# Performance work log

Hardware: AMD Instinct MI355X
Metric: run time of the kernel (lower is better)

Reference implementation:

```python
import jax, jax.numpy as jnp
import numpy as np

EMBED = 256
HEADS = 8
HD = EMBED // HEADS          # head_dim = key_dim = 32 (value_factor=1)
SCALE = HD ** (-0.5)


def angle_transform(x, sin, cos):
    # x: (b, nh, h, w, hd); sin/cos broadcast over leading dims
    x1 = x[..., ::2]
    x2 = x[..., 1::2]
    rot = jnp.stack([-x2, x1], axis=-1).reshape(x.shape)  # interleave (-x2, x1)
    return x * cos + rot * sin


def setup_inputs() -> dict:
    key = jax.random.key(0)
    ks = jax.random.split(key, 12)
    B, H, W = 4, 48, 48
    x = jax.random.normal(ks[0], (B, H, W, EMBED), jnp.float32)
    ang = jax.random.normal(ks[1], (H, W, HD), jnp.float32)
    sin = jnp.sin(ang)
    cos = jnp.cos(ang)
    mask = jax.random.normal(ks[2], (HEADS, H * W, H * W), jnp.float32) * 0.1
    s = 0.05
    Wq = jax.random.normal(ks[3], (EMBED, EMBED), jnp.float32) * s
    bq = jnp.zeros((EMBED,), jnp.float32)
    Wk = jax.random.normal(ks[4], (EMBED, EMBED), jnp.float32) * s
    bk = jnp.zeros((EMBED,), jnp.float32)
    Wv = jax.random.normal(ks[5], (EMBED, EMBED), jnp.float32) * s
    bv = jnp.zeros((EMBED,), jnp.float32)
    lepe_w = jax.random.normal(ks[6], (5, 5, 1, EMBED), jnp.float32) * 0.1  # HWIO, depthwise
    lepe_b = jnp.zeros((EMBED,), jnp.float32)
    Wout = jax.random.normal(ks[7], (EMBED, EMBED), jnp.float32) * s
    bout = jnp.zeros((EMBED,), jnp.float32)
    return {"x": x, "sin": sin, "cos": cos, "mask": mask,
            "Wq": Wq, "bq": bq, "Wk": Wk, "bk": bk, "Wv": Wv, "bv": bv,
            "lepe_w": lepe_w, "lepe_b": lepe_b, "Wout": Wout, "bout": bout}


def reference(x, sin, cos, mask, Wq, bq, Wk, bk, Wv, bv, lepe_w, lepe_b, Wout, bout):
    B, H, W, C = x.shape
    q = x @ Wq + bq
    k = (x @ Wk + bk) * SCALE
    v = x @ Wv + bv
    # depthwise 5x5 conv (lepe) on v, NHWC
    lepe = jax.lax.conv_general_dilated(
        v, lepe_w, window_strides=(1, 1), padding=[(2, 2), (2, 2)],
        dimension_numbers=("NHWC", "HWIO", "NHWC"), feature_group_count=C) + lepe_b
    qh = q.reshape(B, H, W, HEADS, HD).transpose(0, 3, 1, 2, 4)  # (b,nh,h,w,hd)
    kh = k.reshape(B, H, W, HEADS, HD).transpose(0, 3, 1, 2, 4)
    qr = angle_transform(qh, sin, cos).reshape(B, HEADS, H * W, HD)
    kr = angle_transform(kh, sin, cos).reshape(B, HEADS, H * W, HD)
    vr = v.reshape(B, H, W, HEADS, -1).transpose(0, 3, 1, 2, 4).reshape(B, HEADS, H * W, -1)
    attn = jax.nn.softmax(jnp.einsum("bnqd,bnkd->bnqk", qr, kr) + mask, axis=-1)
    out = jnp.einsum("bnqk,bnkd->bnqd", attn, vr)
    out = out.transpose(0, 2, 1, 3).reshape(B, H, W, -1) + lepe
    return out @ Wout + bout
```

## Files before the change

### kernel.cpp

```cpp
#include <hip/hip_runtime.h>
#include <hip/hip_bf16.h>
#include <math.h>

constexpr int kB     = 4;
constexpr int kH     = 48;
constexpr int kW     = 48;
constexpr int kHW    = 2304;
constexpr int kC     = 256;
constexpr int kHeads = 8;
constexpr int kHD    = 32;
constexpr float kScale = 0.17677669529663687f;

typedef __bf16 bf16x8 __attribute__((ext_vector_type(8)));
typedef float  f32x4  __attribute__((ext_vector_type(4)));
typedef unsigned int   uint32x4 __attribute__((ext_vector_type(4)));
typedef unsigned short ushort8v __attribute__((ext_vector_type(8)));

static __device__ __forceinline__ unsigned short f2bf_bits(float f) {
    return __builtin_bit_cast(unsigned short, __float2bfloat16(f));
}

static __device__ __forceinline__ unsigned cvt_pk_bf16(float lo, float hi) {
    unsigned r;
    asm("v_cvt_pk_bf16_f32 %0, %1, %2" : "=v"(r) : "v"(lo), "v"(hi));
    return r;
}

static __device__ __forceinline__ void permlane16_swap(unsigned& a, unsigned& b) {
    asm("v_permlane16_swap_b32 %0, %1" : "+v"(a), "+v"(b));
}
static __device__ __forceinline__ void permlane32_swap(unsigned& a, unsigned& b) {
    asm("v_permlane32_swap_b32 %0, %1" : "+v"(a), "+v"(b));
}

static __device__ __forceinline__ void gll16(const void* g, void* l) {
    __builtin_amdgcn_global_load_lds(
        (const __attribute__((address_space(1))) void*)g,
        (__attribute__((address_space(3))) void*)l, 16, 0, 0);
}

__global__ __launch_bounds__(256) void prep_kernel(
    const float* __restrict__ x,
    const float* __restrict__ Wq, const float* __restrict__ Wk,
    const float* __restrict__ Wv, const float* __restrict__ Wo,
    unsigned short* __restrict__ xb, unsigned short* __restrict__ wt)
{
    const int bid = blockIdx.x;
    if (bid < 2304) {
        const int i = (bid * 256 + threadIdx.x) * 4;
        const float4 v = *reinterpret_cast<const float4*>(x + i);
        alignas(8) unsigned short u[4] = {f2bf_bits(v.x), f2bf_bits(v.y),
                                          f2bf_bits(v.z), f2bf_bits(v.w)};
        *reinterpret_cast<unsigned long long*>(xb + i) =
            *reinterpret_cast<unsigned long long*>(u);
    } else {
        const int e = (bid - 2304) * 256 + threadIdx.x;
        const int m = e >> 16;
        const int r = e & 65535;
        const int k = r >> 8;
        const int n = r & 255;
        const float* W = (m == 0) ? Wq : ((m == 1) ? Wk : ((m == 2) ? Wv : Wo));
        wt[(size_t)m * 65536 + n * 256 + k] = f2bf_bits(W[k * 256 + n]);
    }
}

__global__ __launch_bounds__(256) void qkv_mfma_kernel(
    const unsigned short* __restrict__ xb, const unsigned short* __restrict__ wt,
    const float* __restrict__ bq, const float* __restrict__ bk,
    const float* __restrict__ bv,
    const float* __restrict__ sinb, const float* __restrict__ cosb,
    unsigned short* __restrict__ qbh, unsigned short* __restrict__ kbh,
    unsigned short* __restrict__ vt, float* __restrict__ vb)
{
    const int z = blockIdx.z;
    const unsigned short* wz = wt + (size_t)z * 65536;
    const float* bt = (z == 0) ? bq : ((z == 1) ? bk : bv);
    const int tid  = threadIdx.x;
    const int w    = tid >> 6;
    const int lane = tid & 63;
    const int l    = lane & 15;
    const int g    = lane >> 4;
    const int m0   = blockIdx.x * 64 + w * 16;
    const int nb   = blockIdx.y * 64;

    f32x4 acc[4] = {};
    const unsigned short* xrow = xb + (size_t)(m0 + l) * 256;
    #pragma unroll
    for (int kc = 0; kc < 8; ++kc) {
        const bf16x8 a = *reinterpret_cast<const bf16x8*>(xrow + kc * 32 + g * 8);
        #pragma unroll
        for (int j = 0; j < 4; ++j) {
            const bf16x8 b = *reinterpret_cast<const bf16x8*>(
                wz + (size_t)(nb + 16 * j + l) * 256 + kc * 32 + g * 8);
            acc[j] = __builtin_amdgcn_mfma_f32_16x16x32_bf16(a, b, acc[j], 0, 0, 0);
        }
    }

    int tok[4], bidx[4], hw[4];
    #pragma unroll
    for (int r = 0; r < 4; ++r) {
        tok[r]  = m0 + 4 * g + r;
        bidx[r] = tok[r] / kHW;
        hw[r]   = tok[r] - bidx[r] * kHW;
    }
    const float scl = (z == 1) ? kScale : 1.0f;

    if (z == 2) {
        #pragma unroll
        for (int j = 0; j < 4; ++j) {
            const int c = nb + 16 * j + l;
            const int head = c >> 5, d = c & 31;
            const float bias = bt[c];
            float t[4];
            #pragma unroll
            for (int r = 0; r < 4; ++r) t[r] = acc[j][r] + bias;
            #pragma unroll
            for (int r = 0; r < 4; ++r)
                vb[(((size_t)(bidx[r] * kHeads + head) * kHW + hw[r]) << 5) + d] = t[r];
            alignas(8) unsigned short u[4] = {f2bf_bits(t[0]), f2bf_bits(t[1]),
                                              f2bf_bits(t[2]), f2bf_bits(t[3])};
            *reinterpret_cast<unsigned long long*>(
                vt + ((size_t)(bidx[0] * kHeads + head) * kHD + d) * kHW + hw[0]) =
                *reinterpret_cast<unsigned long long*>(u);
        }
    } else {
        unsigned short* ob = (z == 0) ? qbh : kbh;
        #pragma unroll
        for (int j = 0; j < 4; ++j) {
            const int c = nb + 16 * j + l;
            const int head = c >> 5, d = c & 31;
            const float bias = bt[c];
            float t[4];
            #pragma unroll
            for (int r = 0; r < 4; ++r) t[r] = (acc[j][r] + bias) * scl;
            #pragma unroll
            for (int r = 0; r < 4; ++r) {
                const float p = __shfl_xor(t[r], 1);
                const float cs = cosb[hw[r] * 32 + d];
                const float sn = sinb[hw[r] * 32 + d];
                const float o = (d & 1) ? (t[r] * cs + p * sn)
                                        : (t[r] * cs - p * sn);
                ob[(((size_t)(bidx[r] * kHeads + head) * kHW + hw[r]) << 5) + d] =
                    f2bf_bits(o);
            }
        }
    }
}

__global__ __launch_bounds__(256) void lepe_kernel(
    const float* __restrict__ vb,
    const float* __restrict__ lw, const float* __restrict__ lb,
    float* __restrict__ lepe)
{
    const int c   = threadIdx.x;
    const int bhw = blockIdx.x;
    const int b   = bhw / kHW;
    const int hw  = bhw % kHW;
    const int h   = hw / kW;
    const int w   = hw % kW;
    const int head = c >> 5;
    const int d    = c & 31;

    const float* vsrc = vb + ((size_t)(b * kHeads + head) * kHW) * kHD + d;
    float acc = lb[c];
    #pragma unroll
    for (int dh = 0; dh < 5; ++dh) {
        const int h2 = h + dh - 2;
        if (h2 < 0 || h2 >= kH) continue;
        #pragma unroll
        for (int dw = 0; dw < 5; ++dw) {
            const int w2 = w + dw - 2;
            if (w2 < 0 || w2 >= kW) continue;
            acc += vsrc[(size_t)(h2 * kW + w2) * kHD] * lw[(dh * 5 + dw) * kC + c];
        }
    }
    lepe[(size_t)bhw * kC + c] = acc;
}

__global__ __launch_bounds__(512, 4) void attn_mfma_kernel(
    const __hip_bfloat16* __restrict__ qb, const __hip_bfloat16* __restrict__ kb,
    const __hip_bfloat16* __restrict__ vt, const float* __restrict__ mask,
    float* __restrict__ po, float* __restrict__ ls, int kspan)
{
    extern __shared__ __align__(16) char smem[];
    constexpr int kBufStride = 40960;
    constexpr int kKOff = 8192;
    constexpr int kVOff = 24576;

    const int head = blockIdx.y;
    const int ksl  = blockIdx.z;
    const int tid  = threadIdx.x;
    const int w    = tid >> 6;
    const int b    = w & 3;
    const int sh   = w >> 2;
    const int bh   = b * kHeads + head;
    const int lane = tid & 63;
    const int lq   = lane & 15;
    const int g    = lane >> 4;
    const int q0   = blockIdx.x * 32;
    const int kt0  = ksl * kspan;
    const int nt   = kspan >> 6;
    const bool odd16 = (g & 1);

    const bf16x8 qfrag = *reinterpret_cast<const bf16x8*>(
        reinterpret_cast<const unsigned short*>(qb) +
        ((size_t)bh * kHW + q0 + 16 * sh + lq) * kHD + g * 8);

    const float* msrc;
    {
        const int mrow = w * 4 + (lane >> 4);
        const int mcb  = (lane & 15) ^ (mrow & 7);
        msrc = mask + ((size_t)head * kHW + q0 + mrow) * kHW + kt0 + mcb * 4;
    }
    const unsigned short* kvsrc[4];
    int kvstep, kvregion;
    {
        const unsigned short* kb_bh =
            reinterpret_cast<const unsigned short*>(kb) + (size_t)bh * kHW * kHD;
        const unsigned short* vt_bh =
            reinterpret_cast<const unsigned short*>(vt) + (size_t)bh * kHD * kHW;
        if (sh == 0) {
            #pragma unroll
            for (int i = 0; i < 4; ++i) {
                const int key   = i * 16 + (lane >> 2);
                const int kslot = (lane & 3) ^ (key & 3);
                kvsrc[i] = kb_bh + (size_t)(kt0 + key) * kHD + kslot * 8;
            }
            kvstep = 64 * kHD;
            kvregion = kKOff;
        } else {
            #pragma unroll
            for (int i = 0; i < 4; ++i) {
                const int d   = i * 8 + (lane >> 3);
                const int vcu = (lane & 7) ^ (d & 7);
                kvsrc[i] = vt_bh + (size_t)d * kHW + kt0 + vcu * 8;
            }
            kvstep = 64;
            kvregion = kVOff;
        }
    }

    auto STAGE = [&](int bufo, int tt) {
        gll16(msrc + (size_t)tt * 64, smem + bufo + w * 1024);
        char* kv = smem + bufo + kvregion + b * 4096;
        #pragma unroll
        for (int i = 0; i < 4; ++i)
            gll16(kvsrc[i] + (size_t)tt * kvstep, kv + i * 1024);
    };

    f32x4 o0 = {0.f, 0.f, 0.f, 0.f};
    f32x4 o1 = {0.f, 0.f, 0.f, 0.f};
    float lsum = 0.f;

    const int koff = lq * 64 + ((g ^ (lq & 3)) * 16);
    const int vxa  = (g ^ (lq & 7)) * 16;
    const int vxb  = ((4 + g) ^ (lq & 7)) * 16;

    STAGE(0, 0);

    int cur = 0;
    for (int t = 0; t < nt; ++t) {
        if (t + 1 < nt) {
            STAGE(cur ^ kBufStride, t + 1);
            asm volatile("s_waitcnt vmcnt(5)" ::: "memory");
        } else {
            asm volatile("s_waitcnt vmcnt(0)" ::: "memory");
        }
        __builtin_amdgcn_s_barrier();
        __builtin_amdgcn_sched_barrier(0);

        const char* mb  = smem + cur;
        const char* kbf = smem + cur + kKOff + b * 4096;
        const char* vbf = smem + cur + kVOff + b * 4096;

        bf16x8 kf[4];
        #pragma unroll
        for (int j = 0; j < 4; ++j)
            kf[j] = *reinterpret_cast<const bf16x8*>(kbf + j * 1024 + koff);
        const bf16x8 va  = *reinterpret_cast<const bf16x8*>(vbf + lq * 128 + vxa);
        const bf16x8 vb2 = *reinterpret_cast<const bf16x8*>(vbf + lq * 128 + vxb);
        const bf16x8 vc  = *reinterpret_cast<const bf16x8*>(vbf + (16 + lq) * 128 + vxa);
        const bf16x8 vd  = *reinterpret_cast<const bf16x8*>(vbf + (16 + lq) * 128 + vxb);

        f32x4 st[4];
        #pragma unroll
        for (int j = 0; j < 4; ++j) {
            const f32x4 mc = *reinterpret_cast<const f32x4*>(
                mb + sh * 4096 + lq * 256 + (((4 * j + g) ^ (lq & 7)) * 16));
            st[j] = __builtin_amdgcn_mfma_f32_16x16x32_bf16(kf[j], qfrag, mc, 0, 0, 0);
        }

        unsigned p32[4][2];
        #pragma unroll
        for (int j = 0; j < 4; ++j) {
            const float e0 = __expf(st[j][0]);
            const float e1 = __expf(st[j][1]);
            const float e2 = __expf(st[j][2]);
            const float e3 = __expf(st[j][3]);
            lsum += (e0 + e1) + (e2 + e3);
            p32[j][0] = cvt_pk_bf16(e0, e1);
            p32[j][1] = cvt_pk_bf16(e2, e3);
        }

        unsigned sj[4][2][2];
        #pragma unroll
        for (int j = 0; j < 4; ++j)
            #pragma unroll
            for (int r = 0; r < 2; ++r) {
                unsigned a = p32[j][r], b2 = p32[j][r];
                permlane16_swap(a, b2);
                sj[j][r][0] = a; sj[j][r][1] = b2;
            }
        unsigned pw0[4], pw1[4];
        #pragma unroll
        for (int w2 = 0; w2 < 4; ++w2) {
            const int r = w2 & 1, c = w2 >> 1;
            unsigned pa = sj[0][r][c], pb = sj[1][r][c];
            permlane32_swap(pa, pb);
            pw0[w2] = odd16 ? pb : pa;
            unsigned qa = sj[2][r][c], qb2 = sj[3][r][c];
            permlane32_swap(qa, qb2);
            pw1[w2] = odd16 ? qb2 : qa;
        }
        uint32x4 w0v = {pw0[0], pw0[1], pw0[2], pw0[3]};
        uint32x4 w1v = {pw1[0], pw1[1], pw1[2], pw1[3]};
        const bf16x8 pa0 = __builtin_bit_cast(bf16x8, w0v);
        const bf16x8 pa1 = __builtin_bit_cast(bf16x8, w1v);

        o0 = __builtin_amdgcn_mfma_f32_16x16x32_bf16(pa0, va,  o0, 0, 0, 0);
        o0 = __builtin_amdgcn_mfma_f32_16x16x32_bf16(pa1, vb2, o0, 0, 0, 0);
        o1 = __builtin_amdgcn_mfma_f32_16x16x32_bf16(pa0, vc,  o1, 0, 0, 0);
        o1 = __builtin_amdgcn_mfma_f32_16x16x32_bf16(pa1, vd,  o1, 0, 0, 0);

        asm volatile("s_waitcnt lgkmcnt(0)" ::: "memory");
        __builtin_amdgcn_s_barrier();
        cur ^= kBufStride;
    }

    lsum += __shfl_xor(lsum, 16);
    lsum += __shfl_xor(lsum, 32);

    const size_t pbase = ((size_t)ksl * (kB * kHeads) + bh) * kHW;
    #pragma unroll
    for (int r = 0; r < 4; ++r) {
        float* orow = po + (pbase + q0 + 16 * sh + 4 * g + r) * kHD + lq;
        orow[0]  = o0[r];
        orow[16] = o1[r];
    }
    if (lane < 16) ls[pbase + q0 + 16 * sh + lq] = lsum;
}

__global__ __launch_bounds__(256) void combine_kernel(
    const float* __restrict__ po, const float* __restrict__ ls,
    const float* __restrict__ lepe, unsigned short* __restrict__ abh, int ks)
{
    const int idx = blockIdx.x * 256 + threadIdx.x;
    const int c   = idx & 255;
    const int bhw = idx >> 8;
    const int b   = bhw / kHW;
    const int hw  = bhw % kHW;
    const int head = c >> 5;
    const int d    = c & 31;
    const int bh   = b * kHeads + head;

    float o = 0.f, l = 0.f;
    for (int s = 0; s < ks; ++s) {
        const size_t pbase = ((size_t)s * (kB * kHeads) + bh) * kHW + hw;
        o += po[pbase * kHD + d];
        l += ls[pbase];
    }
    abh[(size_t)idx] = f2bf_bits(o / l + lepe[idx]);
}

__global__ __launch_bounds__(256) void out_mfma_kernel(
    const unsigned short* __restrict__ abh, const unsigned short* __restrict__ wt,
    const float* __restrict__ bo, float* __restrict__ out)
{
    const unsigned short* wz = wt + (size_t)3 * 65536;
    const int tid  = threadIdx.x;
    const int w    = tid >> 6;
    const int lane = tid & 63;
    const int l    = lane & 15;
    const int g    = lane >> 4;
    const int m0   = blockIdx.x * 64 + w * 16;
    const int nb   = blockIdx.y * 64;

    f32x4 acc[4] = {};
    const unsigned short* arow = abh + (size_t)(m0 + l) * 256;
    #pragma unroll
    for (int kc = 0; kc < 8; ++kc) {
        const bf16x8 a = *reinterpret_cast<const bf16x8*>(arow + kc * 32 + g * 8);
        #pragma unroll
        for (int j = 0; j < 4; ++j) {
            const bf16x8 b = *reinterpret_cast<const bf16x8*>(
                wz + (size_t)(nb + 16 * j + l) * 256 + kc * 32 + g * 8);
            acc[j] = __builtin_amdgcn_mfma_f32_16x16x32_bf16(a, b, acc[j], 0, 0, 0);
        }
    }

    #pragma unroll
    for (int j = 0; j < 4; ++j) {
        const int c = nb + 16 * j + l;
        const float bias = bo[c];
        #pragma unroll
        for (int r = 0; r < 4; ++r)
            out[(size_t)(m0 + 4 * g + r) * 256 + c] = acc[j][r] + bias;
    }
}

extern "C" void kernel_launch(void* const* d_in, const int* in_sizes, int n_in,
                              void* d_out, int out_size, void* d_ws, size_t ws_size,
                              hipStream_t stream)
{
    const float* x    = (const float*)d_in[0];
    const float* sinb = (const float*)d_in[1];
    const float* cosb = (const float*)d_in[2];
    const float* mask = (const float*)d_in[3];
    const float* Wq   = (const float*)d_in[4];
    const float* bq   = (const float*)d_in[5];
    const float* Wk   = (const float*)d_in[6];
    const float* bk   = (const float*)d_in[7];
    const float* Wv   = (const float*)d_in[8];
    const float* bv   = (const float*)d_in[9];
    const float* lw   = (const float*)d_in[10];
    const float* lb   = (const float*)d_in[11];
    const float* Wo   = (const float*)d_in[12];
    const float* bo   = (const float*)d_in[13];
    float* out = (float*)d_out;

    const size_t NT = (size_t)kB * kHeads * kHW * kHD;
    const size_t fixed = NT * 4 * 2 + NT * 2 * 5 + 4 * 65536 * 2;

    int ks = 4;
    while (ks > 1) {
        const size_t need = fixed + (size_t)ks * (NT * 4 + (size_t)kB * kHeads * kHW * 4);
        if (need <= ws_size) break;
        ks >>= 1;
    }
    const int kspan = kHW / ks;

    char* base = (char*)d_ws;
    float* vb   = (float*)base;                      base += NT * 4;
    float* lepe = (float*)base;                      base += NT * 4;
    unsigned short* xb  = (unsigned short*)base;     base += NT * 2;
    unsigned short* abh = (unsigned short*)base;     base += NT * 2;
    unsigned short* qbh = (unsigned short*)base;     base += NT * 2;
    unsigned short* kbh = (unsigned short*)base;     base += NT * 2;
    unsigned short* vt  = (unsigned short*)base;     base += NT * 2;
    unsigned short* wt  = (unsigned short*)base;     base += (size_t)4 * 65536 * 2;
    float* po = (float*)base;                        base += (size_t)ks * NT * 4;
    float* ls = (float*)base;                        base += (size_t)ks * kB * kHeads * kHW * 4;

    prep_kernel<<<dim3(3328), 256, 0, stream>>>(x, Wq, Wk, Wv, Wo, xb, wt);
    qkv_mfma_kernel<<<dim3(144, 4, 3), 256, 0, stream>>>(
        xb, wt, bq, bk, bv, sinb, cosb, qbh, kbh, vt, vb);
    lepe_kernel<<<dim3(9216), 256, 0, stream>>>(vb, lw, lb, lepe);
    attn_mfma_kernel<<<dim3(72, 8, ks), 512, 81920, stream>>>(
        (const __hip_bfloat16*)qbh, (const __hip_bfloat16*)kbh,
        (const __hip_bfloat16*)vt, mask, po, ls, kspan);
    combine_kernel<<<dim3(9216), 256, 0, stream>>>(po, ls, lepe, abh, ks);
    out_mfma_kernel<<<dim3(144, 4), 256, 0, stream>>>(abh, wt, bo, out);
}
```

Baseline: 186.5 us.

## Halve attention key tile to 32 and cut LDS, split-K, and raise occupancy

The attention kernel now processes 32 keys per iteration instead of 64, halving the LDS buffer to 40 KB so more blocks can reside per CU (launch bounds raised to 8). Staging is split so one half of the waves loads mask and K while the other loads V, and s_setprio brackets the MFMA section. The split-K factor drops from 4 to 2, which shrinks the partial-output traffic and the combine work but gives each block twice as many iterations. The smaller tile doubles the number of barriers per key processed and gives less MFMA work between them.

Result: slower. 190.6 us (+2.2%).

```diff
diff --git a/kernel.cpp b/kernel.cpp
--- a/kernel.cpp
+++ b/kernel.cpp
@@ -177,15 +177,15 @@
     lepe[(size_t)bhw * kC + c] = acc;
 }
 
-__global__ __launch_bounds__(512, 4) void attn_mfma_kernel(
+__global__ __launch_bounds__(512, 8) void attn_mfma_kernel(
     const __hip_bfloat16* __restrict__ qb, const __hip_bfloat16* __restrict__ kb,
     const __hip_bfloat16* __restrict__ vt, const float* __restrict__ mask,
     float* __restrict__ po, float* __restrict__ ls, int kspan)
 {
     extern __shared__ __align__(16) char smem[];
-    constexpr int kBufStride = 40960;
-    constexpr int kKOff = 8192;
-    constexpr int kVOff = 24576;
+    constexpr int kBufStride = 20480;
+    constexpr int kKOff = 4096;
+    constexpr int kVOff = 12288;
 
     const int head = blockIdx.y;
     const int ksl  = blockIdx.z;
@@ -199,62 +199,60 @@
     const int g    = lane >> 4;
     const int q0   = blockIdx.x * 32;
     const int kt0  = ksl * kspan;
-    const int nt   = kspan >> 6;
+    const int nt   = kspan >> 5;
     const bool odd16 = (g & 1);
 
     const bf16x8 qfrag = *reinterpret_cast<const bf16x8*>(
         reinterpret_cast<const unsigned short*>(qb) +
         ((size_t)bh * kHW + q0 + 16 * sh + lq) * kHD + g * 8);
 
-    const float* msrc;
-    {
-        const int mrow = w * 4 + (lane >> 4);
-        const int mcb  = (lane & 15) ^ (mrow & 7);
-        msrc = mask + ((size_t)head * kHW + q0 + mrow) * kHW + kt0 + mcb * 4;
-    }
-    const unsigned short* kvsrc[4];
-    int kvstep, kvregion;
+    const float* msrc = nullptr;
+    const unsigned short* kvsrc[2];
     {
         const unsigned short* kb_bh =
             reinterpret_cast<const unsigned short*>(kb) + (size_t)bh * kHW * kHD;
         const unsigned short* vt_bh =
             reinterpret_cast<const unsigned short*>(vt) + (size_t)bh * kHD * kHW;
         if (sh == 0) {
-            #pragma unroll
-            for (int i = 0; i < 4; ++i) {
+            const int mrow = w * 8 + (lane >> 3);
+            const int mslot = (lane & 7) ^ (mrow & 7);
+            msrc = mask + ((size_t)head * kHW + q0 + mrow) * kHW + kt0 + mslot * 4;
+            #pragma unroll
+            for (int i = 0; i < 2; ++i) {
                 const int key   = i * 16 + (lane >> 2);
                 const int kslot = (lane & 3) ^ (key & 3);
                 kvsrc[i] = kb_bh + (size_t)(kt0 + key) * kHD + kslot * 8;
             }
-            kvstep = 64 * kHD;
-            kvregion = kKOff;
         } else {
             #pragma unroll
-            for (int i = 0; i < 4; ++i) {
-                const int d   = i * 8 + (lane >> 3);
-                const int vcu = (lane & 7) ^ (d & 7);
-                kvsrc[i] = vt_bh + (size_t)d * kHW + kt0 + vcu * 8;
+            for (int i = 0; i < 2; ++i) {
+                const int d    = i * 16 + (lane >> 2);
+                const int vslot = (lane & 3) ^ (d & 3);
+                kvsrc[i] = vt_bh + (size_t)d * kHW + kt0 + vslot * 8;
             }
-            kvstep = 64;
-            kvregion = kVOff;
         }
     }
 
     auto STAGE = [&](int bufo, int tt) {
-        gll16(msrc + (size_t)tt * 64, smem + bufo + w * 1024);
-        char* kv = smem + bufo + kvregion + b * 4096;
-        #pragma unroll
-        for (int i = 0; i < 4; ++i)
-            gll16(kvsrc[i] + (size_t)tt * kvstep, kv + i * 1024);
+        if (sh == 0) {
+            gll16(msrc + (size_t)tt * 32, smem + bufo + w * 1024);
+            #pragma unroll
+            for (int i = 0; i < 2; ++i)
+                gll16(kvsrc[i] + (size_t)tt * 1024,
+                      smem + bufo + kKOff + b * 2048 + i * 1024);
+        } else {
+            #pragma unroll
+            for (int i = 0; i < 2; ++i)
+                gll16(kvsrc[i] + (size_t)tt * 32,
+                      smem + bufo + kVOff + b * 2048 + i * 1024);
+        }
     };
 
     f32x4 o0 = {0.f, 0.f, 0.f, 0.f};
     f32x4 o1 = {0.f, 0.f, 0.f, 0.f};
     float lsum = 0.f;
 
-    const int koff = lq * 64 + ((g ^ (lq & 3)) * 16);
-    const int vxa  = (g ^ (lq & 7)) * 16;
-    const int vxb  = ((4 + g) ^ (lq & 7)) * 16;
+    const int kvx = (g ^ (lq & 3)) * 16;
 
     STAGE(0, 0);
 
@@ -262,7 +260,8 @@
     for (int t = 0; t < nt; ++t) {
         if (t + 1 < nt) {
             STAGE(cur ^ kBufStride, t + 1);
-            asm volatile("s_waitcnt vmcnt(5)" ::: "memory");
+            if (sh == 0) asm volatile("s_waitcnt vmcnt(3)" ::: "memory");
+            else         asm volatile("s_waitcnt vmcnt(2)" ::: "memory");
         } else {
             asm volatile("s_waitcnt vmcnt(0)" ::: "memory");
         }
@@ -270,29 +269,28 @@
         __builtin_amdgcn_sched_barrier(0);
 
         const char* mb  = smem + cur;
-        const char* kbf = smem + cur + kKOff + b * 4096;
-        const char* vbf = smem + cur + kVOff + b * 4096;
-
-        bf16x8 kf[4];
-        #pragma unroll
-        for (int j = 0; j < 4; ++j)
-            kf[j] = *reinterpret_cast<const bf16x8*>(kbf + j * 1024 + koff);
-        const bf16x8 va  = *reinterpret_cast<const bf16x8*>(vbf + lq * 128 + vxa);
-        const bf16x8 vb2 = *reinterpret_cast<const bf16x8*>(vbf + lq * 128 + vxb);
-        const bf16x8 vc  = *reinterpret_cast<const bf16x8*>(vbf + (16 + lq) * 128 + vxa);
-        const bf16x8 vd  = *reinterpret_cast<const bf16x8*>(vbf + (16 + lq) * 128 + vxb);
-
-        f32x4 st[4];
-        #pragma unroll
-        for (int j = 0; j < 4; ++j) {
+        const char* kbf = smem + cur + kKOff + b * 2048;
+        const char* vbf = smem + cur + kVOff + b * 2048;
+
+        bf16x8 kf[2];
+        #pragma unroll
+        for (int j = 0; j < 2; ++j)
+            kf[j] = *reinterpret_cast<const bf16x8*>(kbf + (16 * j + lq) * 64 + kvx);
+        const bf16x8 va = *reinterpret_cast<const bf16x8*>(vbf + lq * 64 + kvx);
+        const bf16x8 vc = *reinterpret_cast<const bf16x8*>(vbf + (16 + lq) * 64 + kvx);
+
+        __builtin_amdgcn_s_setprio(1);
+        f32x4 st[2];
+        #pragma unroll
+        for (int j = 0; j < 2; ++j) {
             const f32x4 mc = *reinterpret_cast<const f32x4*>(
-                mb + sh * 4096 + lq * 256 + (((4 * j + g) ^ (lq & 7)) * 16));
+                mb + (16 * sh + lq) * 128 + (((4 * j + g) ^ (lq & 7)) * 16));
             st[j] = __builtin_amdgcn_mfma_f32_16x16x32_bf16(kf[j], qfrag, mc, 0, 0, 0);
         }
 
-        unsigned p32[4][2];
-        #pragma unroll
-        for (int j = 0; j < 4; ++j) {
+        unsigned p32[2][2];
+        #pragma unroll
+        for (int j = 0; j < 2; ++j) {
             const float e0 = __expf(st[j][0]);
             const float e1 = __expf(st[j][1]);
             const float e2 = __expf(st[j][2]);
@@ -302,35 +300,29 @@
             p32[j][1] = cvt_pk_bf16(e2, e3);
         }
 
-        unsigned sj[4][2][2];
-        #pragma unroll
-        for (int j = 0; j < 4; ++j)
+        unsigned sj[2][2][2];
+        #pragma unroll
+        for (int j = 0; j < 2; ++j)
             #pragma unroll
             for (int r = 0; r < 2; ++r) {
                 unsigned a = p32[j][r], b2 = p32[j][r];
                 permlane16_swap(a, b2);
                 sj[j][r][0] = a; sj[j][r][1] = b2;
             }
-        unsigned pw0[4], pw1[4];
+        unsigned pw0[4];
         #pragma unroll
         for (int w2 = 0; w2 < 4; ++w2) {
             const int r = w2 & 1, c = w2 >> 1;
             unsigned pa = sj[0][r][c], pb = sj[1][r][c];
             permlane32_swap(pa, pb);
             pw0[w2] = odd16 ? pb : pa;
-            unsigned qa = sj[2][r][c], qb2 = sj[3][r][c];
-            permlane32_swap(qa, qb2);
-            pw1[w2] = odd16 ? qb2 : qa;
         }
         uint32x4 w0v = {pw0[0], pw0[1], pw0[2], pw0[3]};
-        uint32x4 w1v = {pw1[0], pw1[1], pw1[2], pw1[3]};
         const bf16x8 pa0 = __builtin_bit_cast(bf16x8, w0v);
-        const bf16x8 pa1 = __builtin_bit_cast(bf16x8, w1v);
-
-        o0 = __builtin_amdgcn_mfma_f32_16x16x32_bf16(pa0, va,  o0, 0, 0, 0);
-        o0 = __builtin_amdgcn_mfma_f32_16x16x32_bf16(pa1, vb2, o0, 0, 0, 0);
-        o1 = __builtin_amdgcn_mfma_f32_16x16x32_bf16(pa0, vc,  o1, 0, 0, 0);
-        o1 = __builtin_amdgcn_mfma_f32_16x16x32_bf16(pa1, vd,  o1, 0, 0, 0);
+
+        o0 = __builtin_amdgcn_mfma_f32_16x16x32_bf16(pa0, va, o0, 0, 0, 0);
+        o1 = __builtin_amdgcn_mfma_f32_16x16x32_bf16(pa0, vc, o1, 0, 0, 0);
+        __builtin_amdgcn_s_setprio(0);
 
         asm volatile("s_waitcnt lgkmcnt(0)" ::: "memory");
         __builtin_amdgcn_s_barrier();
@@ -431,7 +423,7 @@
     const size_t NT = (size_t)kB * kHeads * kHW * kHD;
     const size_t fixed = NT * 4 * 2 + NT * 2 * 5 + 4 * 65536 * 2;
 
-    int ks = 4;
+    int ks = 2;
     while (ks > 1) {
         const size_t need = fixed + (size_t)ks * (NT * 4 + (size_t)kB * kHeads * kHW * 4);
         if (need <= ws_size) break;
@@ -455,7 +447,7 @@
     qkv_mfma_kernel<<<dim3(144, 4, 3), 256, 0, stream>>>(
         xb, wt, bq, bk, bv, sinb, cosb, qbh, kbh, vt, vb);
     lepe_kernel<<<dim3(9216), 256, 0, stream>>>(vb, lw, lb, lepe);
-    attn_mfma_kernel<<<dim3(72, 8, ks), 512, 81920, stream>>>(
+    attn_mfma_kernel<<<dim3(72, 8, ks), 512, 40960, stream>>>(
         (const __hip_bfloat16*)qbh, (const __hip_bfloat16*)kbh,
         (const __hip_bfloat16*)vt, mask, po, ls, kspan);
     combine_kernel<<<dim3(9216), 256, 0, stream>>>(po, ls, lepe, abh, ks);
```

## Fuse split-K combine into output projection and reduce attention key splits

Applied to the files above, without the earlier changes.

Removes the separate combine kernel. The output-projection GEMM now reads the partial attention outputs and row sums directly, normalizes them, adds lepe, and packs to bf16 in registers. The output kernel tile widens to 128 columns, the split-K count drops from 4 to 2, and the attention MFMA section gets raised wave priority. The aim is to drop a kernel launch and the abh round trip through memory. In exchange, the partial data is re-read across the column blocks, and fewer key splits means less attention parallelism.

Result: no change. 190.2 us (+2.0%).

```diff
diff --git a/kernel.cpp b/kernel.cpp
--- a/kernel.cpp
+++ b/kernel.cpp
@@ -282,6 +282,7 @@
         const bf16x8 vc  = *reinterpret_cast<const bf16x8*>(vbf + (16 + lq) * 128 + vxa);
         const bf16x8 vd  = *reinterpret_cast<const bf16x8*>(vbf + (16 + lq) * 128 + vxb);
 
+        __builtin_amdgcn_s_setprio(1);
         f32x4 st[4];
         #pragma unroll
         for (int j = 0; j < 4; ++j) {
@@ -331,6 +332,7 @@
         o0 = __builtin_amdgcn_mfma_f32_16x16x32_bf16(pa1, vb2, o0, 0, 0, 0);
         o1 = __builtin_amdgcn_mfma_f32_16x16x32_bf16(pa0, vc,  o1, 0, 0, 0);
         o1 = __builtin_amdgcn_mfma_f32_16x16x32_bf16(pa1, vd,  o1, 0, 0, 0);
+        __builtin_amdgcn_s_setprio(0);
 
         asm volatile("s_waitcnt lgkmcnt(0)" ::: "memory");
         __builtin_amdgcn_s_barrier();
@@ -350,31 +352,10 @@
     if (lane < 16) ls[pbase + q0 + 16 * sh + lq] = lsum;
 }
 
-__global__ __launch_bounds__(256) void combine_kernel(
+__global__ __launch_bounds__(256, 4) void out_mfma_kernel(
     const float* __restrict__ po, const float* __restrict__ ls,
-    const float* __restrict__ lepe, unsigned short* __restrict__ abh, int ks)
-{
-    const int idx = blockIdx.x * 256 + threadIdx.x;
-    const int c   = idx & 255;
-    const int bhw = idx >> 8;
-    const int b   = bhw / kHW;
-    const int hw  = bhw % kHW;
-    const int head = c >> 5;
-    const int d    = c & 31;
-    const int bh   = b * kHeads + head;
-
-    float o = 0.f, l = 0.f;
-    for (int s = 0; s < ks; ++s) {
-        const size_t pbase = ((size_t)s * (kB * kHeads) + bh) * kHW + hw;
-        o += po[pbase * kHD + d];
-        l += ls[pbase];
-    }
-    abh[(size_t)idx] = f2bf_bits(o / l + lepe[idx]);
-}
-
-__global__ __launch_bounds__(256) void out_mfma_kernel(
-    const unsigned short* __restrict__ abh, const unsigned short* __restrict__ wt,
-    const float* __restrict__ bo, float* __restrict__ out)
+    const float* __restrict__ lepe, const unsigned short* __restrict__ wt,
+    const float* __restrict__ bo, float* __restrict__ out, int ks)
 {
     const unsigned short* wz = wt + (size_t)3 * 65536;
     const int tid  = threadIdx.x;
@@ -383,23 +364,58 @@
     const int l    = lane & 15;
     const int g    = lane >> 4;
     const int m0   = blockIdx.x * 64 + w * 16;
-    const int nb   = blockIdx.y * 64;
-
-    f32x4 acc[4] = {};
-    const unsigned short* arow = abh + (size_t)(m0 + l) * 256;
+    const int nb   = blockIdx.y * 128;
+
+    const int tok = m0 + l;
+    const int b   = tok / kHW;
+    const int hw  = tok - b * kHW;
+    const int bh0 = b * kHeads;
+
+    float rinv[8];
+    #pragma unroll
+    for (int h = 0; h < 8; ++h) {
+        float s = ls[((size_t)0 * 32 + bh0 + h) * kHW + hw];
+        if (ks > 1) s += ls[((size_t)1 * 32 + bh0 + h) * kHW + hw];
+        rinv[h] = 1.0f / s;
+    }
+
+    f32x4 acc[8] = {};
     #pragma unroll
     for (int kc = 0; kc < 8; ++kc) {
-        const bf16x8 a = *reinterpret_cast<const bf16x8*>(arow + kc * 32 + g * 8);
-        #pragma unroll
-        for (int j = 0; j < 4; ++j) {
-            const bf16x8 b = *reinterpret_cast<const bf16x8*>(
+        const float* p0 = po + (((size_t)0 * 32 + bh0 + kc) * kHW + hw) * kHD + g * 8;
+        f32x4 sA = *reinterpret_cast<const f32x4*>(p0);
+        f32x4 sB = *reinterpret_cast<const f32x4*>(p0 + 4);
+        if (ks > 1) {
+            const float* p1 = po + (((size_t)1 * 32 + bh0 + kc) * kHW + hw) * kHD + g * 8;
+            const f32x4 tA = *reinterpret_cast<const f32x4*>(p1);
+            const f32x4 tB = *reinterpret_cast<const f32x4*>(p1 + 4);
+            #pragma unroll
+            for (int i = 0; i < 4; ++i) { sA[i] += tA[i]; sB[i] += tB[i]; }
+        }
+        const float* le = lepe + (size_t)tok * 256 + kc * 32 + g * 8;
+        const f32x4 lA = *reinterpret_cast<const f32x4*>(le);
+        const f32x4 lB = *reinterpret_cast<const f32x4*>(le + 4);
+        const float ri = rinv[kc];
+        float av[8];
+        #pragma unroll
+        for (int i = 0; i < 4; ++i) {
+            av[i]     = sA[i] * ri + lA[i];
+            av[i + 4] = sB[i] * ri + lB[i];
+        }
+        uint32x4 ap = {cvt_pk_bf16(av[0], av[1]), cvt_pk_bf16(av[2], av[3]),
+                       cvt_pk_bf16(av[4], av[5]), cvt_pk_bf16(av[6], av[7])};
+        const bf16x8 a = __builtin_bit_cast(bf16x8, ap);
+
+        #pragma unroll
+        for (int j = 0; j < 8; ++j) {
+            const bf16x8 bfr = *reinterpret_cast<const bf16x8*>(
                 wz + (size_t)(nb + 16 * j + l) * 256 + kc * 32 + g * 8);
-            acc[j] = __builtin_amdgcn_mfma_f32_16x16x32_bf16(a, b, acc[j], 0, 0, 0);
-        }
-    }
-
-    #pragma unroll
-    for (int j = 0; j < 4; ++j) {
+            acc[j] = __builtin_amdgcn_mfma_f32_16x16x32_bf16(a, bfr, acc[j], 0, 0, 0);
+        }
+    }
+
+    #pragma unroll
+    for (int j = 0; j < 8; ++j) {
         const int c = nb + 16 * j + l;
         const float bias = bo[c];
         #pragma unroll
@@ -429,9 +445,9 @@
     float* out = (float*)d_out;
 
     const size_t NT = (size_t)kB * kHeads * kHW * kHD;
-    const size_t fixed = NT * 4 * 2 + NT * 2 * 5 + 4 * 65536 * 2;
-
-    int ks = 4;
+    const size_t fixed = NT * 4 * 2 + NT * 2 * 4 + 4 * 65536 * 2;
+
+    int ks = 2;
     while (ks > 1) {
         const size_t need = fixed + (size_t)ks * (NT * 4 + (size_t)kB * kHeads * kHW * 4);
         if (need <= ws_size) break;
@@ -443,7 +459,6 @@
     float* vb   = (float*)base;                      base += NT * 4;
     float* lepe = (float*)base;                      base += NT * 4;
     unsigned short* xb  = (unsigned short*)base;     base += NT * 2;
-    unsigned short* abh = (unsigned short*)base;     base += NT * 2;
     unsigned short* qbh = (unsigned short*)base;     base += NT * 2;
     unsigned short* kbh = (unsigned short*)base;     base += NT * 2;
     unsigned short* vt  = (unsigned short*)base;     base += NT * 2;
@@ -458,6 +473,6 @@
     attn_mfma_kernel<<<dim3(72, 8, ks), 512, 81920, stream>>>(
         (const __hip_bfloat16*)qbh, (const __hip_bfloat16*)kbh,
         (const __hip_bfloat16*)vt, mask, po, ls, kspan);
-    combine_kernel<<<dim3(9216), 256, 0, stream>>>(po, ls, lepe, abh, ks);
-    out_mfma_kernel<<<dim3(144, 4), 256, 0, stream>>>(abh, wt, bo, out);
-}
+    out_mfma_kernel<<<dim3(144, 2), 256, 0, stream>>>(
+        po, ls, lepe, wt, bo, out, ks);
+}
```
